# Performance work log

Hardware: AMD Instinct MI355X
Metric: run time of the kernel (lower is better)

The kernel has to match this reference:

```python
import jax, jax.numpy as jnp
import numpy as np
from jax import lax

TOP_K = 2

def _unfold(x_img, k):
    # F.unfold(kernel=k, stride=k): [B,C,H,W] -> [B, C*k*k, L], column index c*k*k + kh*k + kw
    B, C, H, W = x_img.shape
    Hp, Wp = H // k, W // k
    u = x_img.reshape(B, C, Hp, k, Wp, k).transpose(0, 1, 3, 5, 2, 4)
    return u.reshape(B, C * k * k, Hp * Wp)

def _fold(p, k, H, W):
    # F.fold inverse of non-overlapping unfold: [B, C*k*k, L] -> [B,C,H,W]
    B = p.shape[0]
    C = p.shape[1] // (k * k)
    Hp, Wp = H // k, W // k
    u = p.reshape(B, C, k, k, Hp, Wp).transpose(0, 1, 4, 2, 5, 3)
    return u.reshape(B, C, H, W)

def setup_inputs() -> dict:
    key = jax.random.key(0)
    ks = jax.random.split(key, 6)
    B, H, W, C, F, E, P = 8, 64, 64, 384, 1536, 8, 4
    N = H * W
    x = jax.random.normal(ks[0], (B, N, C), dtype=jnp.float32)
    gate_w = jax.random.normal(ks[1], (E, C, P, P), dtype=jnp.float32) * 0.01
    w1 = jax.random.normal(ks[2], (E, C, F), dtype=jnp.float32) * (1.0 / np.sqrt(C))
    b1 = jax.random.normal(ks[3], (E, F), dtype=jnp.float32) * 0.01
    w2 = jax.random.normal(ks[4], (E, F, C), dtype=jnp.float32) * (1.0 / np.sqrt(F))
    b2 = jax.random.normal(ks[5], (E, C), dtype=jnp.float32) * 0.01
    return {"x": x, "gate_w": gate_w, "w1": w1, "b1": b1, "w2": w2, "b2": b2, "H": H, "W": W}

def reference(x, gate_w, w1, b1, w2, b2, H, W):
    B, N, C = x.shape
    E, _, P, _ = gate_w.shape
    k2 = P * P
    Hp, Wp = H // P, W // P
    L = Hp * Wp
    x_img = jnp.transpose(x, (0, 2, 1)).reshape(B, C, H, W)
    # router: strided conv -> logits per patch
    logits_map = lax.conv_general_dilated(
        x_img, gate_w, window_strides=(P, P), padding='VALID',
        dimension_numbers=('NCHW', 'OIHW', 'NCHW'))  # [B,E,Hp,Wp]
    router_logits = jnp.transpose(logits_map, (0, 2, 3, 1)).reshape(B, L, E)
    probs = jax.nn.softmax(router_logits, axis=-1)
    ew, ei = lax.top_k(probs, TOP_K)  # [B,L,topk]
    ew = ew / (jnp.sum(ew, axis=-1, keepdims=True) + 1e-9)
    # expand to token level (faithful to original's reshape/flatten ordering)
    ei_tok = jnp.broadcast_to(ei[:, :, None, :], (B, L, k2, TOP_K)).reshape(-1, TOP_K)
    ew_tok = jnp.broadcast_to(ew[:, :, None, :], (B, L, k2, TOP_K)).reshape(-1, TOP_K)
    # unfold + the original's (scrambled) reshape(B, C, L, k2)
    U = _unfold(x_img, P)  # [B, C*k2, L]
    x_patches = jnp.transpose(U.reshape(B, C, L, k2), (0, 2, 3, 1))  # [B,L,k2,C]
    flat_x = x_patches.reshape(-1, C)  # [T,C], T = B*L*k2
    # combine weights: zero for experts not in top-k == masked dispatch math
    cw = jnp.zeros((flat_x.shape[0], E), dtype=flat_x.dtype)
    for kk in range(TOP_K):
        cw = cw + jax.nn.one_hot(ei_tok[:, kk], E, dtype=flat_x.dtype) * ew_tok[:, kk:kk + 1]
    out = jnp.zeros_like(flat_x)
    for e in range(E):
        h = jax.nn.gelu(flat_x @ w1[e] + b1[e], approximate=False)
        y = h @ w2[e] + b2[e]
        out = out + cw[:, e:e + 1] * y
    # fold back (mirrors original's reshape/permute exactly)
    o = jnp.transpose(out.reshape(B, L, k2, C), (0, 3, 1, 2)).reshape(B, C * k2, L)
    out_img = _fold(o, P, H, W)  # [B,C,H,W]
    # original: output.transpose(1,2).reshape(B,N,C) on NCHW tensor
    output = jnp.transpose(out_img, (0, 2, 1, 3)).reshape(B, N, C)
    return output
```

## Files before the change

kernel.cpp:

```cpp
#include <hip/hip_runtime.h>
#include <hip/hip_bf16.h>

#define BB   8
#define HH   64
#define WWID 64
#define CC   384
#define FF   1536
#define EE   8
#define LL   256
#define MTOTMAX 66560
#define NTMAX   520

typedef unsigned short ushort_t;
typedef __attribute__((ext_vector_type(4))) unsigned short u16x4;
typedef __attribute__((ext_vector_type(8))) short          s16x8;
typedef __attribute__((ext_vector_type(4))) float          f32x4;

__device__ __forceinline__ float bf2f(ushort_t u) {
  union { unsigned int i; float f; } v; v.i = ((unsigned int)u) << 16; return v.f;
}
__device__ __forceinline__ ushort_t f2bf(float f) {
  union { float f; unsigned int i; } v; v.f = f;
  unsigned int u = v.i;
  u += 0x7fffu + ((u >> 16) & 1u);
  return (ushort_t)(u >> 16);
}
__device__ __forceinline__ float gelu_f(float x) {
  float u  = 0.70710678118654752f * x;
  float au = fabsf(u);
  float t  = 1.0f / (1.0f + 0.3275911f * au);
  float poly = t * (0.254829592f + t * (-0.284496736f + t * (1.421413741f +
               t * (-1.453152027f + t * 1.061405429f))));
  float ea = 1.0f - poly * __expf(-au * au);
  float erfv = (x < 0.f) ? -ea : ea;
  return 0.5f * x * (1.0f + erfv);
}

#define GLDS(g, l) __builtin_amdgcn_global_load_lds( \
    (const __attribute__((address_space(1))) void*)(g), \
    (__attribute__((address_space(3))) void*)(l), 16, 0, 0)

__global__ __launch_bounds__(256) void k_transpose(const float* __restrict__ src,
                                                   ushort_t* __restrict__ dst,
                                                   int R, int Cd) {
  __shared__ ushort_t tile[32][33];
  int e  = blockIdx.z;
  int c0 = blockIdx.x * 32, r0 = blockIdx.y * 32;
  int tx = threadIdx.x & 31, ty = threadIdx.x >> 5;
  const float* s = src + (size_t)e * R * Cd;
  ushort_t*    d = dst + (size_t)e * R * Cd;
  #pragma unroll
  for (int i = 0; i < 32; i += 8)
    tile[ty + i][tx] = f2bf(s[(size_t)(r0 + ty + i) * Cd + c0 + tx]);
  __syncthreads();
  #pragma unroll
  for (int i = 0; i < 32; i += 8)
    d[(size_t)(c0 + ty + i) * R + r0 + tx] = tile[tx][ty + i];
}

__global__ void k_tgw(const float* __restrict__ gw, float* __restrict__ gwt) {
  int e = blockIdx.x, t = threadIdx.x;
  for (int i = t; i < CC * 16; i += 256) {
    int c = i >> 4, p = i & 15;
    gwt[((size_t)e * 16 + p) * CC + c] = gw[(size_t)e * CC * 16 + i];
  }
}

__global__ __launch_bounds__(256) void k_router(const float* __restrict__ x,
                                                const float* __restrict__ gwt,
                                                int* __restrict__ re, float* __restrict__ rw,
                                                int* __restrict__ cnt) {
  int bid = blockIdx.x;
  int b = bid >> 8, l2 = bid & 255;
  int hp = l2 >> 4, wp = l2 & 15;
  int t = threadIdx.x;
  int e = t >> 5, lane = t & 31;
  const float* xb = x + (size_t)b * (HH * WWID) * CC;
  const float* ge = gwt + (size_t)e * 16 * CC;
  float acc = 0.f;
  #pragma unroll
  for (int p = 0; p < 16; ++p) {
    int pix = (hp * 4 + (p >> 2)) * 64 + wp * 4 + (p & 3);
    const float* xr = xb + (size_t)pix * CC;
    const float* gr = ge + (size_t)p * CC;
    #pragma unroll
    for (int it = 0; it < 3; ++it) {
      f32x4 xv = *reinterpret_cast<const f32x4*>(xr + it * 128 + lane * 4);
      f32x4 gv = *reinterpret_cast<const f32x4*>(gr + it * 128 + lane * 4);
      acc += xv.x * gv.x + xv.y * gv.y + xv.z * gv.z + xv.w * gv.w;
    }
  }
  #pragma unroll
  for (int d = 16; d; d >>= 1) acc += __shfl_down(acc, d, 32);
  __shared__ float logits[EE];
  if (lane == 0) logits[e] = acc;
  __syncthreads();
  if (t == 0) {
    float m = logits[0];
    #pragma unroll
    for (int i = 1; i < EE; ++i) m = fmaxf(m, logits[i]);
    float p[EE]; float s = 0.f;
    #pragma unroll
    for (int i = 0; i < EE; ++i) { p[i] = __expf(logits[i] - m); s += p[i]; }
    #pragma unroll
    for (int i = 0; i < EE; ++i) p[i] /= s;
    int e0 = 0;
    #pragma unroll
    for (int i = 1; i < EE; ++i) if (p[i] > p[e0]) e0 = i;
    int e1 = (e0 == 0) ? 1 : 0;
    #pragma unroll
    for (int i = 0; i < EE; ++i) if (i != e0 && p[i] > p[e1]) e1 = i;
    float s2 = p[e0] + p[e1] + 1e-9f;
    re[bid * 2 + 0] = e0;  re[bid * 2 + 1] = e1;
    rw[bid * 2 + 0] = p[e0] / s2;  rw[bid * 2 + 1] = p[e1] / s2;
    atomicAdd(&cnt[e0], 16);
    atomicAdd(&cnt[e1], 16);
  }
}

__global__ void k_pad(const int* __restrict__ cnt, int* __restrict__ cntp,
                      int* __restrict__ basep, int* __restrict__ tile2e,
                      int* __restrict__ gids, float* __restrict__ gwts) {
  __shared__ int s_cnt[EE], s_cntp[EE], s_base[EE + 1];
  int t = threadIdx.x;
  if (t == 0) {
    int b = 0;
    for (int e = 0; e < EE; ++e) {
      int c  = cnt[e];
      int cp = (c + 127) & ~127;
      s_cnt[e] = c; s_cntp[e] = cp; s_base[e] = b;
      b += cp;
    }
    s_base[EE] = b;
  }
  __syncthreads();
  if (t < EE) { cntp[t] = s_cntp[t]; basep[t] = s_base[t]; }
  if (t == EE) basep[EE] = s_base[EE];
  int ntot = s_base[EE] >> 7;
  for (int g = t; g < ntot; g += 256) {
    int e = 0;
    #pragma unroll
    for (int i = 1; i < EE; ++i) if (g * 128 >= s_base[i]) e = i;
    tile2e[g] = e;
  }
  for (int e = 0; e < EE; ++e)
    for (int i = s_cnt[e] + t; i < s_cntp[e]; i += 256) {
      gids[s_base[e] + i] = -1;
      gwts[s_base[e] + i] = 0.f;
    }
}

__global__ void k_assign(const int* __restrict__ re, const float* __restrict__ rw,
                         const int* __restrict__ basep, int* __restrict__ cnt2,
                         int* __restrict__ gids, float* __restrict__ gwts,
                         int* __restrict__ inv) {
  int i = blockIdx.x * blockDim.x + threadIdx.x;
  if (i >= BB * LL * 2) return;
  int pat = i >> 1, slot = i & 1;
  int b = pat >> 8, l2 = pat & 255;
  int e = re[i];
  float w = rw[i];
  int t2 = l2 >> 4, hp = l2 & 15;
  int kh = t2 >> 2, kw = t2 & 3;
  int h = hp * 4 + kh;
  int row = basep[e] + atomicAdd(&cnt2[e], 16);
  #pragma unroll
  for (int j = 0; j < 16; ++j) {
    int wpix = j * 4 + kw;
    int pix = (b << 12) + (h << 6) + wpix;
    gids[row + j] = pix;
    gwts[row + j] = w;
    inv[(slot << 15) + pix] = row + j;
  }
}

__global__ __launch_bounds__(256) void k_gather(const float* __restrict__ x,
                                                const int* __restrict__ gids,
                                                const int* __restrict__ basep,
                                                ushort_t* __restrict__ Xc, int t0) {
  int g = t0 + blockIdx.x;
  if (g * 128 >= basep[EE]) return;
  __shared__ int s_id[128];
  int t = threadIdx.x;
  if (t < 128) s_id[t] = gids[g * 128 + t];
  __syncthreads();
  ushort_t* dst = Xc + (size_t)blockIdx.x * 128 * CC;
  for (int i = t; i < 128 * 96; i += 256) {
    int row = i / 96, ch = (i % 96) * 4;
    int id = s_id[row];
    f32x4 v = (f32x4){0.f, 0.f, 0.f, 0.f};
    if (id >= 0) v = *reinterpret_cast<const f32x4*>(x + (size_t)(id & 32767) * CC + ch);
    u16x4 o = {f2bf(v.x), f2bf(v.y), f2bf(v.z), f2bf(v.w)};
    *reinterpret_cast<u16x4*>(dst + (size_t)row * CC + ch) = o;
  }
}

__global__ __launch_bounds__(256, 3) void k_gemm1(const ushort_t* __restrict__ Xc,
                                                  const ushort_t* __restrict__ w1t,
                                                  const float* __restrict__ b1,
                                                  const int* __restrict__ basep,
                                                  const int* __restrict__ tile2e,
                                                  ushort_t* __restrict__ Hc, int t0) {
  int g = t0 + blockIdx.y;
  if (g * 128 >= basep[EE]) return;
  int e = tile2e[g], fg = blockIdx.x;
  __shared__ ushort_t As[12 * 512];
  __shared__ ushort_t Bs[8 * 512];
  int t = threadIdx.x, w = t >> 6, lane = t & 63;
  int l15 = lane & 15, q = lane >> 4;
  const ushort_t* a_src = w1t + ((size_t)e * FF + fg * 192) * CC;
  const ushort_t* b_src = Xc + (size_t)blockIdx.y * 128 * CC;
  f32x4 acc[6][4];
  #pragma unroll
  for (int i = 0; i < 6; ++i)
    #pragma unroll
    for (int j = 0; j < 4; ++j) acc[i][j] = (f32x4){0.f, 0.f, 0.f, 0.f};

  for (int k0 = 0; k0 < CC; k0 += 32) {
    __syncthreads();
    #pragma unroll
    for (int c = 0; c < 5; ++c) {
      int ch = w * 5 + c;
      if (ch < 12) GLDS(a_src + (size_t)(ch * 16 + l15) * CC + k0 + q * 8, As + ch * 512);
      else         GLDS(b_src + (size_t)((ch - 12) * 16 + l15) * CC + k0 + q * 8, Bs + (ch - 12) * 512);
    }
    __syncthreads();
    s16x8 af[6], bf[4];
    #pragma unroll
    for (int i = 0; i < 6; ++i)
      af[i] = *reinterpret_cast<const s16x8*>(As + ((w & 1) * 6 + i) * 512 + lane * 8);
    #pragma unroll
    for (int j = 0; j < 4; ++j)
      bf[j] = *reinterpret_cast<const s16x8*>(Bs + ((w >> 1) * 4 + j) * 512 + lane * 8);
    #pragma unroll
    for (int i = 0; i < 6; ++i)
      #pragma unroll
      for (int j = 0; j < 4; ++j)
        acc[i][j] = __builtin_amdgcn_mfma_f32_16x16x32_bf16(af[i], bf[j], acc[i][j], 0, 0, 0);
  }

  ushort_t* hbase = Hc + (size_t)blockIdx.y * 128 * FF;
  int fb = fg * 192 + (w & 1) * 96 + q * 4;
  f32x4 bias[6];
  #pragma unroll
  for (int i = 0; i < 6; ++i)
    bias[i] = *reinterpret_cast<const f32x4*>(b1 + (size_t)e * FF + fb + i * 16);
  #pragma unroll
  for (int j = 0; j < 4; ++j) {
    int m = (w >> 1) * 64 + j * 16 + l15;
    ushort_t* hp = hbase + (size_t)m * FF + fb;
    #pragma unroll
    for (int i = 0; i < 6; ++i) {
      u16x4 v;
      #pragma unroll
      for (int r = 0; r < 4; ++r)
        v[r] = f2bf(gelu_f(acc[i][j][r] + bias[i][r]));
      *reinterpret_cast<u16x4*>(hp + i * 16) = v;
    }
  }
}

__global__ __launch_bounds__(256, 3) void k_gemm2(const ushort_t* __restrict__ Hc,
                                                  const ushort_t* __restrict__ w2t,
                                                  const float* __restrict__ b2,
                                                  const int* __restrict__ basep,
                                                  const int* __restrict__ tile2e,
                                                  const float* __restrict__ gwts,
                                                  ushort_t* __restrict__ y, int t0) {
  int g = t0 + blockIdx.y;
  if (g * 128 >= basep[EE]) return;
  int e = tile2e[g], nb = blockIdx.x;
  __shared__ ushort_t As[12 * 512];
  __shared__ ushort_t Bs[8 * 512];
  __shared__ float s_w[128];
  int t = threadIdx.x, w = t >> 6, lane = t & 63;
  int l15 = lane & 15, q = lane >> 4;
  if (t < 128) s_w[t] = gwts[g * 128 + t];
  const ushort_t* a_src = w2t + ((size_t)e * CC + nb * 192) * FF;
  const ushort_t* b_src = Hc + (size_t)blockIdx.y * 128 * FF;
  f32x4 acc[6][4];
  #pragma unroll
  for (int i = 0; i < 6; ++i)
    #pragma unroll
    for (int j = 0; j < 4; ++j) acc[i][j] = (f32x4){0.f, 0.f, 0.f, 0.f};

  for (int k0 = 0; k0 < FF; k0 += 32) {
    __syncthreads();
    #pragma unroll
    for (int c = 0; c < 5; ++c) {
      int ch = w * 5 + c;
      if (ch < 12) GLDS(a_src + (size_t)(ch * 16 + l15) * FF + k0 + q * 8, As + ch * 512);
      else         GLDS(b_src + (size_t)((ch - 12) * 16 + l15) * FF + k0 + q * 8, Bs + (ch - 12) * 512);
    }
    __syncthreads();
    s16x8 af[6], bf[4];
    #pragma unroll
    for (int i = 0; i < 6; ++i)
      af[i] = *reinterpret_cast<const s16x8*>(As + ((w & 1) * 6 + i) * 512 + lane * 8);
    #pragma unroll
    for (int j = 0; j < 4; ++j)
      bf[j] = *reinterpret_cast<const s16x8*>(Bs + ((w >> 1) * 4 + j) * 512 + lane * 8);
    #pragma unroll
    for (int i = 0; i < 6; ++i)
      #pragma unroll
      for (int j = 0; j < 4; ++j)
        acc[i][j] = __builtin_amdgcn_mfma_f32_16x16x32_bf16(af[i], bf[j], acc[i][j], 0, 0, 0);
  }

  int cb = nb * 192 + (w & 1) * 96 + q * 4;
  f32x4 bias[6];
  #pragma unroll
  for (int i = 0; i < 6; ++i)
    bias[i] = *reinterpret_cast<const f32x4*>(b2 + (size_t)e * CC + cb + i * 16);
  ushort_t* ybase = y + (size_t)g * 128 * CC;
  #pragma unroll
  for (int j = 0; j < 4; ++j) {
    int m = (w >> 1) * 64 + j * 16 + l15;
    float wt = s_w[m];
    ushort_t* yp = ybase + (size_t)m * CC + cb;
    #pragma unroll
    for (int i = 0; i < 6; ++i) {
      u16x4 v;
      #pragma unroll
      for (int r = 0; r < 4; ++r)
        v[r] = f2bf((acc[i][j][r] + bias[i][r]) * wt);
      *reinterpret_cast<u16x4*>(yp + i * 16) = v;
    }
  }
}

__global__ __launch_bounds__(256) void k_final(const ushort_t* __restrict__ y,
                                               const int* __restrict__ inv,
                                               float* __restrict__ out) {
  int bid = blockIdx.x;
  __shared__ float tile[64][193];
  __shared__ int s_r0[64], s_r1[64];
  int t = threadIdx.x;
  if (t < 64) {
    s_r0[t] = inv[(bid << 6) + t];
    s_r1[t] = inv[32768 + (bid << 6) + t];
  }
  __syncthreads();
  float* dst = out + (size_t)bid * CC * WWID;
  #pragma unroll
  for (int half = 0; half < 2; ++half) {
    int c0 = half * 192;
    for (int i = t; i < 64 * 48; i += 256) {
      int w = i / 48, c4 = (i % 48) * 4;
      u16x4 a = *reinterpret_cast<const u16x4*>(y + (size_t)s_r0[w] * CC + c0 + c4);
      u16x4 b = *reinterpret_cast<const u16x4*>(y + (size_t)s_r1[w] * CC + c0 + c4);
      #pragma unroll
      for (int k = 0; k < 4; ++k)
        tile[w][c4 + k] = bf2f(a[k]) + bf2f(b[k]);
    }
    __syncthreads();
    for (int i = t; i < 64 * 192; i += 256) {
      int cl = i / 64, w = i % 64;
      dst[(size_t)(c0 + cl) * WWID + w] = tile[w][cl];
    }
    __syncthreads();
  }
}

extern "C" void kernel_launch(void* const* d_in, const int* in_sizes, int n_in,
                              void* d_out, int out_size, void* d_ws, size_t ws_size,
                              hipStream_t stream) {
  const float* x  = (const float*)d_in[0];
  const float* gw = (const float*)d_in[1];
  const float* w1 = (const float*)d_in[2];
  const float* b1 = (const float*)d_in[3];
  const float* w2 = (const float*)d_in[4];
  const float* b2 = (const float*)d_in[5];

  const size_t fixed = (size_t)EE * FF * CC * 2 * 2
                     + (size_t)MTOTMAX * CC * 2
                     + (size_t)EE * 16 * CC * 4
                     + (size_t)MTOTMAX * 4 * 2
                     + (size_t)65536 * 4
                     + (size_t)BB * LL * 2 * 4 * 2
                     + (size_t)NTMAX * 4
                     + 1024;
  const int cands[6] = {32768, 16384, 8192, 4096, 2048, 1024};
  int MC = 1024;
  for (int i = 0; i < 6; ++i)
    if (fixed + (size_t)cands[i] * 3840 <= ws_size) { MC = cands[i]; break; }
  const int npass = (MTOTMAX + MC - 1) / MC;
  const int ntile = MC / 128;

  char* ws = (char*)d_ws;
  size_t off = 0;
  ushort_t* Xc   = (ushort_t*)(ws + off); off += (size_t)MC * CC * 2;
  ushort_t* Hc   = (ushort_t*)(ws + off); off += (size_t)MC * FF * 2;
  ushort_t* w1t  = (ushort_t*)(ws + off); off += (size_t)EE * FF * CC * 2;
  ushort_t* w2t  = (ushort_t*)(ws + off); off += (size_t)EE * FF * CC * 2;
  ushort_t* y    = (ushort_t*)(ws + off); off += (size_t)MTOTMAX * CC * 2;
  float* gwt   = (float*)(ws + off); off += (size_t)EE * 16 * CC * 4;
  int*   gids  = (int*)(ws + off);   off += (size_t)MTOTMAX * 4;
  float* gwts  = (float*)(ws + off); off += (size_t)MTOTMAX * 4;
  int*   inv   = (int*)(ws + off);   off += (size_t)65536 * 4;
  int*   re    = (int*)(ws + off);   off += (size_t)BB * LL * 2 * 4;
  float* rw    = (float*)(ws + off); off += (size_t)BB * LL * 2 * 4;
  int*   tile2e= (int*)(ws + off);   off += (size_t)NTMAX * 4;
  int*   cnt   = (int*)(ws + off);   off += 64;
  int*   cnt2  = (int*)(ws + off);   off += 64;
  int*   cntp  = (int*)(ws + off);   off += 64;
  int*   basep = (int*)(ws + off);   off += 64;

  hipMemsetAsync(cnt, 0, 128, stream);

  k_transpose<<<dim3(FF / 32, CC / 32, EE), 256, 0, stream>>>(w1, w1t, CC, FF);
  k_transpose<<<dim3(CC / 32, FF / 32, EE), 256, 0, stream>>>(w2, w2t, FF, CC);
  k_tgw<<<EE, 256, 0, stream>>>(gw, gwt);
  k_router<<<BB * LL, 256, 0, stream>>>(x, gwt, re, rw, cnt);
  k_pad<<<1, 256, 0, stream>>>(cnt, cntp, basep, tile2e, gids, gwts);
  k_assign<<<16, 256, 0, stream>>>(re, rw, basep, cnt2, gids, gwts, inv);

  for (int p = 0; p < npass; ++p) {
    int t0 = p * ntile;
    k_gather<<<ntile, 256, 0, stream>>>(x, gids, basep, Xc, t0);
    k_gemm1<<<dim3(FF / 192, ntile), 256, 0, stream>>>(Xc, w1t, b1, basep, tile2e, Hc, t0);
    k_gemm2<<<dim3(CC / 192, ntile), 256, 0, stream>>>(Hc, w2t, b2, basep, tile2e, gwts, y, t0);
  }
  k_final<<<BB * HH, 256, 0, stream>>>(y, inv, (float*)d_out);
}
```

Measured before the change: 698.7 us.

## Double-buffer LDS in expert GEMMs with unified 128x128 templated kernel

Merges the two expert GEMM kernels into one template and shrinks the output tile from 192x128 to 128x128. The k-loop now uses two LDS buffers, so the global-to-LDS load for the next k-slice is issued while MFMAs run on the current one, and it needs one barrier per step instead of two. It also raises wave priority around the MFMA block and asks for 4 blocks per CU. The smaller tile means more blocks and more operand reloads per FLOP, traded against better latency hiding and occupancy.

```diff
diff --git a/kernel.cpp b/kernel.cpp
--- a/kernel.cpp
+++ b/kernel.cpp
@@ -195,136 +195,97 @@
   }
 }
 
-__global__ __launch_bounds__(256, 3) void k_gemm1(const ushort_t* __restrict__ Xc,
-                                                  const ushort_t* __restrict__ w1t,
-                                                  const float* __restrict__ b1,
-                                                  const int* __restrict__ basep,
-                                                  const int* __restrict__ tile2e,
-                                                  ushort_t* __restrict__ Hc, int t0) {
+#define GSTEP(RD, ST, KNEXT, DOST)                                            \
+  {                                                                           \
+    if (DOST) {                                                               \
+      _Pragma("unroll")                                                       \
+      for (int c = 0; c < 4; ++c)                                             \
+        GLDS(src_c[c] + (KNEXT), (ST) + (w * 4 + c) * 512);                   \
+    }                                                                         \
+    s16x8 af[4], bf[4];                                                       \
+    _Pragma("unroll")                                                         \
+    for (int i = 0; i < 4; ++i)                                               \
+      af[i] = *reinterpret_cast<const s16x8*>((RD) + ((w & 1) * 4 + i) * 512 + lane * 8); \
+    _Pragma("unroll")                                                         \
+    for (int j = 0; j < 4; ++j)                                               \
+      bf[j] = *reinterpret_cast<const s16x8*>((RD) + (8 + (w >> 1) * 4 + j) * 512 + lane * 8); \
+    __builtin_amdgcn_s_setprio(1);                                            \
+    _Pragma("unroll")                                                         \
+    for (int i = 0; i < 4; ++i)                                               \
+      _Pragma("unroll")                                                       \
+      for (int j = 0; j < 4; ++j)                                             \
+        acc[i][j] = __builtin_amdgcn_mfma_f32_16x16x32_bf16(af[i], bf[j], acc[i][j], 0, 0, 0); \
+    __builtin_amdgcn_s_setprio(0);                                            \
+    __syncthreads();                                                          \
+  }
+
+template<int K, int NOUT, bool GELU, bool OUTG>
+__global__ __launch_bounds__(256, 4) void k_gemm(const ushort_t* __restrict__ A,
+                                                 const ushort_t* __restrict__ Bsrc,
+                                                 const float* __restrict__ bias,
+                                                 const int* __restrict__ basep,
+                                                 const int* __restrict__ tile2e,
+                                                 const float* __restrict__ gwts,
+                                                 ushort_t* __restrict__ out, int t0) {
   int g = t0 + blockIdx.y;
   if (g * 128 >= basep[EE]) return;
-  int e = tile2e[g], fg = blockIdx.x;
-  __shared__ ushort_t As[12 * 512];
-  __shared__ ushort_t Bs[8 * 512];
-  int t = threadIdx.x, w = t >> 6, lane = t & 63;
-  int l15 = lane & 15, q = lane >> 4;
-  const ushort_t* a_src = w1t + ((size_t)e * FF + fg * 192) * CC;
-  const ushort_t* b_src = Xc + (size_t)blockIdx.y * 128 * CC;
-  f32x4 acc[6][4];
-  #pragma unroll
-  for (int i = 0; i < 6; ++i)
-    #pragma unroll
-    for (int j = 0; j < 4; ++j) acc[i][j] = (f32x4){0.f, 0.f, 0.f, 0.f};
-
-  for (int k0 = 0; k0 < CC; k0 += 32) {
-    __syncthreads();
-    #pragma unroll
-    for (int c = 0; c < 5; ++c) {
-      int ch = w * 5 + c;
-      if (ch < 12) GLDS(a_src + (size_t)(ch * 16 + l15) * CC + k0 + q * 8, As + ch * 512);
-      else         GLDS(b_src + (size_t)((ch - 12) * 16 + l15) * CC + k0 + q * 8, Bs + (ch - 12) * 512);
-    }
-    __syncthreads();
-    s16x8 af[6], bf[4];
-    #pragma unroll
-    for (int i = 0; i < 6; ++i)
-      af[i] = *reinterpret_cast<const s16x8*>(As + ((w & 1) * 6 + i) * 512 + lane * 8);
-    #pragma unroll
-    for (int j = 0; j < 4; ++j)
-      bf[j] = *reinterpret_cast<const s16x8*>(Bs + ((w >> 1) * 4 + j) * 512 + lane * 8);
-    #pragma unroll
-    for (int i = 0; i < 6; ++i)
-      #pragma unroll
-      for (int j = 0; j < 4; ++j)
-        acc[i][j] = __builtin_amdgcn_mfma_f32_16x16x32_bf16(af[i], bf[j], acc[i][j], 0, 0, 0);
-  }
-
-  ushort_t* hbase = Hc + (size_t)blockIdx.y * 128 * FF;
-  int fb = fg * 192 + (w & 1) * 96 + q * 4;
-  f32x4 bias[6];
-  #pragma unroll
-  for (int i = 0; i < 6; ++i)
-    bias[i] = *reinterpret_cast<const f32x4*>(b1 + (size_t)e * FF + fb + i * 16);
-  #pragma unroll
-  for (int j = 0; j < 4; ++j) {
-    int m = (w >> 1) * 64 + j * 16 + l15;
-    ushort_t* hp = hbase + (size_t)m * FF + fb;
-    #pragma unroll
-    for (int i = 0; i < 6; ++i) {
-      u16x4 v;
-      #pragma unroll
-      for (int r = 0; r < 4; ++r)
-        v[r] = f2bf(gelu_f(acc[i][j][r] + bias[i][r]));
-      *reinterpret_cast<u16x4*>(hp + i * 16) = v;
-    }
-  }
-}
-
-__global__ __launch_bounds__(256, 3) void k_gemm2(const ushort_t* __restrict__ Hc,
-                                                  const ushort_t* __restrict__ w2t,
-                                                  const float* __restrict__ b2,
-                                                  const int* __restrict__ basep,
-                                                  const int* __restrict__ tile2e,
-                                                  const float* __restrict__ gwts,
-                                                  ushort_t* __restrict__ y, int t0) {
-  int g = t0 + blockIdx.y;
-  if (g * 128 >= basep[EE]) return;
-  int e = tile2e[g], nb = blockIdx.x;
-  __shared__ ushort_t As[12 * 512];
-  __shared__ ushort_t Bs[8 * 512];
+  int e = tile2e[g], ng = blockIdx.x;
+  __shared__ ushort_t S[2][16 * 512];
   __shared__ float s_w[128];
   int t = threadIdx.x, w = t >> 6, lane = t & 63;
   int l15 = lane & 15, q = lane >> 4;
-  if (t < 128) s_w[t] = gwts[g * 128 + t];
-  const ushort_t* a_src = w2t + ((size_t)e * CC + nb * 192) * FF;
-  const ushort_t* b_src = Hc + (size_t)blockIdx.y * 128 * FF;
-  f32x4 acc[6][4];
-  #pragma unroll
-  for (int i = 0; i < 6; ++i)
+  if (!GELU && t < 128) s_w[t] = gwts[g * 128 + t];
+  const ushort_t* a_src = A + ((size_t)e * NOUT + ng * 128) * K;
+  const ushort_t* b_src = Bsrc + (size_t)blockIdx.y * 128 * K;
+
+  const ushort_t* src_c[4];
+  #pragma unroll
+  for (int c = 0; c < 4; ++c) {
+    int ch = w * 4 + c;
+    src_c[c] = (ch < 8)
+      ? a_src + (size_t)(ch * 16 + l15) * K + q * 8
+      : b_src + (size_t)((ch - 8) * 16 + l15) * K + q * 8;
+  }
+
+  f32x4 acc[4][4];
+  #pragma unroll
+  for (int i = 0; i < 4; ++i)
     #pragma unroll
     for (int j = 0; j < 4; ++j) acc[i][j] = (f32x4){0.f, 0.f, 0.f, 0.f};
 
-  for (int k0 = 0; k0 < FF; k0 += 32) {
-    __syncthreads();
-    #pragma unroll
-    for (int c = 0; c < 5; ++c) {
-      int ch = w * 5 + c;
-      if (ch < 12) GLDS(a_src + (size_t)(ch * 16 + l15) * FF + k0 + q * 8, As + ch * 512);
-      else         GLDS(b_src + (size_t)((ch - 12) * 16 + l15) * FF + k0 + q * 8, Bs + (ch - 12) * 512);
-    }
-    __syncthreads();
-    s16x8 af[6], bf[4];
-    #pragma unroll
-    for (int i = 0; i < 6; ++i)
-      af[i] = *reinterpret_cast<const s16x8*>(As + ((w & 1) * 6 + i) * 512 + lane * 8);
-    #pragma unroll
-    for (int j = 0; j < 4; ++j)
-      bf[j] = *reinterpret_cast<const s16x8*>(Bs + ((w >> 1) * 4 + j) * 512 + lane * 8);
-    #pragma unroll
-    for (int i = 0; i < 6; ++i)
-      #pragma unroll
-      for (int j = 0; j < 4; ++j)
-        acc[i][j] = __builtin_amdgcn_mfma_f32_16x16x32_bf16(af[i], bf[j], acc[i][j], 0, 0, 0);
-  }
-
-  int cb = nb * 192 + (w & 1) * 96 + q * 4;
-  f32x4 bias[6];
-  #pragma unroll
-  for (int i = 0; i < 6; ++i)
-    bias[i] = *reinterpret_cast<const f32x4*>(b2 + (size_t)e * CC + cb + i * 16);
-  ushort_t* ybase = y + (size_t)g * 128 * CC;
+  ushort_t* S0 = &S[0][0];
+  ushort_t* S1 = &S[1][0];
+
+  #pragma unroll
+  for (int c = 0; c < 4; ++c) GLDS(src_c[c], S0 + (w * 4 + c) * 512);
+  __syncthreads();
+
+  constexpr int NIT = K / 32;
+  for (int it = 0; it < NIT; it += 2) {
+    GSTEP(S0, S1, (size_t)(it + 1) * 32, true);
+    GSTEP(S1, S0, (size_t)(it + 2) * 32, it + 2 < NIT);
+  }
+
+  int nb = ng * 128 + (w & 1) * 64 + q * 4;
+  f32x4 bv[4];
+  #pragma unroll
+  for (int i = 0; i < 4; ++i)
+    bv[i] = *reinterpret_cast<const f32x4*>(bias + (size_t)e * NOUT + nb + i * 16);
+  ushort_t* ob = out + (OUTG ? (size_t)g : (size_t)blockIdx.y) * 128 * NOUT;
   #pragma unroll
   for (int j = 0; j < 4; ++j) {
     int m = (w >> 1) * 64 + j * 16 + l15;
-    float wt = s_w[m];
-    ushort_t* yp = ybase + (size_t)m * CC + cb;
-    #pragma unroll
-    for (int i = 0; i < 6; ++i) {
+    float wt = GELU ? 1.f : s_w[m];
+    ushort_t* op = ob + (size_t)m * NOUT + nb;
+    #pragma unroll
+    for (int i = 0; i < 4; ++i) {
       u16x4 v;
       #pragma unroll
-      for (int r = 0; r < 4; ++r)
-        v[r] = f2bf((acc[i][j][r] + bias[i][r]) * wt);
-      *reinterpret_cast<u16x4*>(yp + i * 16) = v;
+      for (int r = 0; r < 4; ++r) {
+        float xv = acc[i][j][r] + bv[i][r];
+        v[r] = f2bf(GELU ? gelu_f(xv) : xv * wt);
+      }
+      *reinterpret_cast<u16x4*>(op + i * 16) = v;
     }
   }
 }
@@ -418,8 +379,10 @@
   for (int p = 0; p < npass; ++p) {
     int t0 = p * ntile;
     k_gather<<<ntile, 256, 0, stream>>>(x, gids, basep, Xc, t0);
-    k_gemm1<<<dim3(FF / 192, ntile), 256, 0, stream>>>(Xc, w1t, b1, basep, tile2e, Hc, t0);
-    k_gemm2<<<dim3(CC / 192, ntile), 256, 0, stream>>>(Hc, w2t, b2, basep, tile2e, gwts, y, t0);
+    k_gemm<CC, FF, true,  false><<<dim3(FF / 128, ntile), 256, 0, stream>>>(
+        w1t, Xc, b1, basep, tile2e, (const float*)nullptr, Hc, t0);
+    k_gemm<FF, CC, false, true ><<<dim3(CC / 128, ntile), 256, 0, stream>>>(
+        w2t, Hc, b2, basep, tile2e, gwts, y, t0);
   }
   k_final<<<BB * HH, 256, 0, stream>>>(y, inv, (float*)d_out);
 }
```

Result: no change. 696.3 us (-0.3%).
